# Kernel tuning notes

Hardware: AMD Instinct MI355X
Metric: run time of the kernel (lower is better)

## Reference

```python
import jax, jax.numpy as jnp
import numpy as np

N = 50000  # num_nodes
K_DIFF = 2  # max_diffusion_step


def _spmm(rows, cols, vals, x):
    # sparse (N,N) @ dense (N,F): y[r] += v * x[c]
    return jax.ops.segment_sum(vals[:, None] * x[cols], rows, num_segments=N)


def setup_inputs() -> dict:
    key = jax.random.key(0)
    ks = jax.random.split(key, 9)
    B, D, O, E = 8, 64, 64, 1600000
    num_matrices = 2 * K_DIFF + 1
    return {
        "x": jax.random.normal(ks[0], (B, N, D), dtype=jnp.float32),
        "rows0": jax.random.randint(ks[1], (E,), 0, N),
        "cols0": jax.random.randint(ks[2], (E,), 0, N),
        "vals0": jax.random.uniform(ks[3], (E,), dtype=jnp.float32),
        "rows1": jax.random.randint(ks[4], (E,), 0, N),
        "cols1": jax.random.randint(ks[5], (E,), 0, N),
        "vals1": jax.random.uniform(ks[6], (E,), dtype=jnp.float32),
        "weight": jax.random.normal(ks[7], (D * num_matrices, O), dtype=jnp.float32) * 0.1,
        "biases": jnp.zeros((O,), dtype=jnp.float32),
    }


def reference(x, rows0, cols0, vals0, rows1, cols1, vals1, weight, biases):
    B, n, D = x.shape
    # 'b n d -> n (b d)'
    x0 = jnp.transpose(x, (1, 0, 2)).reshape(n, B * D)
    xs = [x0]
    for (r, c, v) in ((rows0, cols0, vals0), (rows1, cols1, vals1)):
        x1 = _spmm(r, c, v, x0)
        xs.append(x1)
        x_prev, x_curr = x0, x1
        for _ in range(2, K_DIFF + 1):
            x_next = 2.0 * _spmm(r, c, v, x_curr) - x_prev
            xs.append(x_next)
            x_prev, x_curr = x_curr, x_next
    Km = len(xs)
    xk = jnp.stack(xs, axis=0).reshape(Km, n, B, D)  # k n b d
    # 'k n (b d) -> b n d k' then '(b n)(d k)'
    feat = jnp.transpose(xk, (2, 1, 3, 0)).reshape(B * n, D * Km)
    out = feat @ weight + biases
    return out.reshape(B, n, -1)
```

## Files before the change

kernel.cpp:

```cpp
#include <hip/hip_runtime.h>

#define N_NODES 50000
#define BDIM 8
#define DDIM 64
#define ODIM 64
#define KM 5
#define BD 512
#define CAP 72
#define CAPL 76
#define YSTR 88
#define SCHUNKS 8
#define CROWS (N_NODES / SCHUNKS)
#define SLICES 8
#define SFEAT 64
#define RBLK_H ((N_NODES + 31) / 32)

typedef unsigned int u32;
typedef unsigned short u16;

typedef __attribute__((ext_vector_type(8))) short short8;
typedef __attribute__((ext_vector_type(4))) float f32x4;

__device__ __forceinline__ u16 pack1(float f) {
  u32 a = __float_as_uint(f);
  return (u16)((a + 0x7FFFu + ((a >> 16) & 1u)) >> 16);
}
__device__ __forceinline__ u32 pack2(float f0, float f1) {
  return (u32)pack1(f0) | ((u32)pack1(f1) << 16);
}
__device__ __forceinline__ float bfl(u32 u) { return __uint_as_float(u << 16); }
__device__ __forceinline__ float bfh(u32 u) { return __uint_as_float(u & 0xFFFF0000u); }

__device__ __forceinline__ int wave_max(int v) {
  v = max(v, __shfl_xor(v, 8));
  v = max(v, __shfl_xor(v, 16));
  v = max(v, __shfl_xor(v, 32));
  return v;
}

__global__ void k_transpose_h(const float* __restrict__ x, u16* __restrict__ x0h, int tot4) {
  int i = blockIdx.x * blockDim.x + threadIdx.x;
  if (i >= tot4) return;
  int f = i << 2;
  int d = f & (DDIM - 1);
  int nb = f >> 6;
  int b = nb / N_NODES;
  int n = nb - b * N_NODES;
  float4 v = *(const float4*)(x + (size_t)f);
  uint2 w = make_uint2(pack2(v.x, v.y), pack2(v.z, v.w));
  *(uint2*)(x0h + (size_t)n * BD + b * DDIM + d) = w;
}

__global__ void __launch_bounds__(256) k_scatter_cap(
    const int* __restrict__ r0, const int* __restrict__ c0, const float* __restrict__ v0,
    const int* __restrict__ r1, const int* __restrict__ c1, const float* __restrict__ v1,
    int* __restrict__ cnt , u32* __restrict__ cv , int E4, int bpc) {
  int chunk = blockIdx.x / bpc;
  int i = (blockIdx.x - chunk * bpc) * blockDim.x + threadIdx.x;
  int lo = chunk * CROWS;
  const int* rr; const int* cc; const float* vv; int base, j;
  if (i < E4) { rr = r0; cc = c0; vv = v0; base = 0; j = i; }
  else if (i < 2 * E4) { rr = r1; cc = c1; vv = v1; base = N_NODES; j = i - E4; }
  else return;
  int4 r = *(const int4*)(rr + (size_t)j * 4);
  int4 c = *(const int4*)(cc + (size_t)j * 4);
  float4 v = *(const float4*)(vv + (size_t)j * 4);
  int p;
  if ((u32)(r.x - lo) < CROWS) {
    p = atomicAdd(&cnt[base + r.x], 1);
    if (p < CAP) cv[(size_t)(base + r.x) * CAP + p] = (u32)c.x | ((u32)pack1(v.x) << 16);
  }
  if ((u32)(r.y - lo) < CROWS) {
    p = atomicAdd(&cnt[base + r.y], 1);
    if (p < CAP) cv[(size_t)(base + r.y) * CAP + p] = (u32)c.y | ((u32)pack1(v.y) << 16);
  }
  if ((u32)(r.z - lo) < CROWS) {
    p = atomicAdd(&cnt[base + r.z], 1);
    if (p < CAP) cv[(size_t)(base + r.z) * CAP + p] = (u32)c.z | ((u32)pack1(v.z) << 16);
  }
  if ((u32)(r.w - lo) < CROWS) {
    p = atomicAdd(&cnt[base + r.w], 1);
    if (p < CAP) cv[(size_t)(base + r.w) * CAP + p] = (u32)c.w | ((u32)pack1(v.w) << 16);
  }
}

__global__ void k_prep_w(const float* __restrict__ weight, u16* __restrict__ wfrag) {
  for (int i = threadIdx.x; i < 2560; i += 256) {
    int lane = i & 63;
    int ob = (i >> 6) & 3;
    int half = (i >> 8) & 1;
    int k = i >> 9;
    int o = ob * 16 + (lane & 15);
    #pragma unroll
    for (int j = 0; j < 8; ++j) {
      int d = half * 32 + ((lane >> 4) * 8) + j;
      wfrag[(size_t)i * 8 + j] = pack1(weight[(d * KM + k) * ODIM + o]);
    }
  }
}

__device__ __forceinline__ const short8* wfp(const u16* __restrict__ wfrag,
                                             int k, int h, int ob, int lane) {
  return (const short8*)(wfrag + (size_t)((((k * 2 + h) * 4 + ob) * 64 + lane) * 8));
}

__device__ __forceinline__ void fma8(float a[8], uint4 q, float v) {
  a[0] = fmaf(v, bfl(q.x), a[0]); a[1] = fmaf(v, bfh(q.x), a[1]);
  a[2] = fmaf(v, bfl(q.y), a[2]); a[3] = fmaf(v, bfh(q.y), a[3]);
  a[4] = fmaf(v, bfl(q.z), a[4]); a[5] = fmaf(v, bfh(q.z), a[5]);
  a[6] = fmaf(v, bfl(q.w), a[6]); a[7] = fmaf(v, bfh(q.w), a[7]);
}

__device__ __forceinline__ void gather_lds(const u32* __restrict__ cvp ,
                                           const u16* __restrict__ xb,
                                           int n, int nmax, float acc[8]) {
  float A0[8] = {}, A1[8] = {}, A2[8] = {}, A3[8] = {};
  int e = 0;
  for (; e + 4 <= nmax; e += 4) {
    uint4 q = *(const uint4*)(cvp + e);
    u32 q0 = (e + 0 < n) ? q.x : 0u;
    u32 q1 = (e + 1 < n) ? q.y : 0u;
    u32 q2 = (e + 2 < n) ? q.z : 0u;
    u32 q3 = (e + 3 < n) ? q.w : 0u;
    uint4 d0 = *(const uint4*)(xb + (size_t)(q0 & 0xFFFFu) * BD);
    uint4 d1 = *(const uint4*)(xb + (size_t)(q1 & 0xFFFFu) * BD);
    uint4 d2 = *(const uint4*)(xb + (size_t)(q2 & 0xFFFFu) * BD);
    uint4 d3 = *(const uint4*)(xb + (size_t)(q3 & 0xFFFFu) * BD);
    fma8(A0, d0, bfh(q0));
    fma8(A1, d1, bfh(q1));
    fma8(A2, d2, bfh(q2));
    fma8(A3, d3, bfh(q3));
  }
  for (; e < nmax; ++e) {
    u32 q = (e < n) ? cvp[e] : 0u;
    uint4 d = *(const uint4*)(xb + (size_t)(q & 0xFFFFu) * BD);
    fma8(A0, d, bfh(q));
  }
  #pragma unroll
  for (int j = 0; j < 8; ++j) acc[j] = (A0[j] + A1[j]) + (A2[j] + A3[j]);
}

template<int G>
__device__ __forceinline__ void stage_cv(const int* __restrict__ cnt, const u32* __restrict__ cv,
                                         int rbase, u32* __restrict__ cvl, int* __restrict__ nn) {
  if (threadIdx.x < 32 * G) {
    int g = threadIdx.x >> 5, i2 = threadIdx.x & 31;
    int node = rbase + i2;
    nn[threadIdx.x] = (node < N_NODES) ? min(cnt[g * N_NODES + node], CAP) : 0;
  }
  const int QR = CAP / 4;
  for (int idx = threadIdx.x; idx < G * 32 * QR; idx += 256) {
    int g = idx / (32 * QR);
    int rem = idx - g * (32 * QR);
    int i2 = rem / QR, w = rem - i2 * QR;
    int node = rbase + i2;
    uint4 q = (node < N_NODES)
        ? *(const uint4*)(cv + (size_t)(g * N_NODES + node) * CAP + w * 4)
        : make_uint4(0, 0, 0, 0);
    *(uint4*)(&cvl[(g * 32 + i2) * CAPL + w * 4]) = q;
  }
  __syncthreads();
}

__global__ void __launch_bounds__(256, 4) k_hop1f(const int* __restrict__ cnt,
                                                  const u32* __restrict__ cv,
                                                  const u16* __restrict__ x0h,
                                                  const u16* __restrict__ wfrag,
                                                  const float* __restrict__ bias,
                                                  u16* __restrict__ slabA0,
                                                  u16* __restrict__ slabA1,
                                                  float* __restrict__ out) {
  __shared__ u32 cvl[2 * 32 * CAPL];
  __shared__ int nn[64];
  const int sid = blockIdx.x / RBLK_H;
  const int rbase = (blockIdx.x - sid * RBLK_H) * 32;
  stage_cv<2>(cnt, cv, rbase, cvl, nn);

  const int wid = threadIdx.x >> 6, lane = threadIdx.x & 63;
  const int gi = lane >> 3, pe = lane & 7;
  const int i2 = wid * 8 + gi;
  const int node = rbase + i2;
  const bool nv = node < N_NODES;
  const int n0 = nn[i2], n1 = nn[32 + i2];
  const int m0 = wave_max(n0), m1 = wave_max(n1);
  const u32* cvp0 = &cvl[i2 * CAPL];
  const u32* cvp1 = &cvl[(32 + i2) * CAPL];

  const int t = wid >> 1, obp = (wid & 1) * 2;
  const int ar = lane & 15, kg = lane >> 4, col = lane & 15;
  const int anode = min(rbase + t * 16 + ar, N_NODES - 1);
  const float bv0 = bias[obp * 16 + col];
  const float bv1 = bias[(obp + 1) * 16 + col];

  for (int s = sid * 4; s < sid * 4 + 4; ++s) {
    const u16* xb = x0h + s * SFEAT + pe * 8;
    float y0[8], y1[8];
    gather_lds(cvp0, xb, n0, m0, y0);
    gather_lds(cvp1, xb, n1, m1, y1);
    if (nv) {
      size_t doff = (size_t)node * BD + s * SFEAT + pe * 8;
      *(uint4*)(slabA0 + doff) = make_uint4(pack2(y0[0], y0[1]), pack2(y0[2], y0[3]),
                                            pack2(y0[4], y0[5]), pack2(y0[6], y0[7]));
      *(uint4*)(slabA1 + doff) = make_uint4(pack2(y1[0], y1[1]), pack2(y1[2], y1[3]),
                                            pack2(y1[4], y1[5]), pack2(y1[6], y1[7]));
    }
    f32x4 acc0 = {0.f, 0.f, 0.f, 0.f}, acc1 = {0.f, 0.f, 0.f, 0.f};
    #pragma unroll
    for (int h = 0; h < 2; ++h) {
      short8 a = *(const short8*)(x0h + (size_t)anode * BD + s * SFEAT + h * 32 + kg * 8);
      acc0 = __builtin_amdgcn_mfma_f32_16x16x32_bf16(a, *wfp(wfrag, 0, h, obp, lane), acc0, 0, 0, 0);
      acc1 = __builtin_amdgcn_mfma_f32_16x16x32_bf16(a, *wfp(wfrag, 0, h, obp + 1, lane), acc1, 0, 0, 0);
    }
    #pragma unroll
    for (int reg = 0; reg < 4; ++reg) {
      int onode = rbase + t * 16 + kg * 4 + reg;
      if (onode < N_NODES) {
        size_t ob_ = ((size_t)s * N_NODES + onode) * ODIM;
        out[ob_ + obp * 16 + col] = acc0[reg] + bv0;
        out[ob_ + (obp + 1) * 16 + col] = acc1[reg] + bv1;
      }
    }
  }
}

template<int KSELF, int KY>
__global__ void __launch_bounds__(256, 4) k_hop2(const int* __restrict__ cnt_g,
                                                 const u32* __restrict__ cv_g,
                                                 const u16* __restrict__ srcslab,
                                                 const u16* __restrict__ x0h,
                                                 const u16* __restrict__ wfrag,
                                                 float* __restrict__ out) {
  __shared__ u32 cvl[32 * CAPL];
  __shared__ int nn[32];
  __shared__ u16 ytile[32 * YSTR];
  const int sid = blockIdx.x / RBLK_H;
  const int rbase = (blockIdx.x - sid * RBLK_H) * 32;
  stage_cv<1>(cnt_g, cv_g, rbase, cvl, nn);

  const int wid = threadIdx.x >> 6, lane = threadIdx.x & 63;
  const int gi = lane >> 3, pe = lane & 7;
  const int i2 = wid * 8 + gi;
  const int node = rbase + i2;
  const int nsafe = min(node, N_NODES - 1);
  const int n = nn[i2];
  const int m = wave_max(n);
  const u32* cvp = &cvl[i2 * CAPL];

  const int t = wid >> 1, obp = (wid & 1) * 2;
  const int ar = lane & 15, kg = lane >> 4, col = lane & 15;
  const int anode = min(rbase + t * 16 + ar, N_NODES - 1);

  for (int s = sid * 4; s < sid * 4 + 4; ++s) {
    const u16* xb = srcslab + s * SFEAT + pe * 8;
    float y[8];
    gather_lds(cvp, xb, n, m, y);
    {
      uint4 qp = *(const uint4*)(x0h + (size_t)nsafe * BD + s * SFEAT + pe * 8);
      float p[8] = {bfl(qp.x), bfh(qp.x), bfl(qp.y), bfh(qp.y),
                    bfl(qp.z), bfh(qp.z), bfl(qp.w), bfh(qp.w)};
      #pragma unroll
      for (int j = 0; j < 8; ++j) y[j] = 2.f * y[j] - p[j];
    }
    *(uint4*)(&ytile[i2 * YSTR + pe * 8]) =
        make_uint4(pack2(y[0], y[1]), pack2(y[2], y[3]),
                   pack2(y[4], y[5]), pack2(y[6], y[7]));
    __syncthreads();
    f32x4 acc0 = {0.f, 0.f, 0.f, 0.f}, acc1 = {0.f, 0.f, 0.f, 0.f};
    #pragma unroll
    for (int h = 0; h < 2; ++h) {
      short8 aS = *(const short8*)(srcslab + (size_t)anode * BD + s * SFEAT + h * 32 + kg * 8);
      short8 aY = *(const short8*)(&ytile[(t * 16 + ar) * YSTR + h * 32 + kg * 8]);
      acc0 = __builtin_amdgcn_mfma_f32_16x16x32_bf16(aS, *wfp(wfrag, KSELF, h, obp, lane), acc0, 0, 0, 0);
      acc1 = __builtin_amdgcn_mfma_f32_16x16x32_bf16(aS, *wfp(wfrag, KSELF, h, obp + 1, lane), acc1, 0, 0, 0);
      acc0 = __builtin_amdgcn_mfma_f32_16x16x32_bf16(aY, *wfp(wfrag, KY, h, obp, lane), acc0, 0, 0, 0);
      acc1 = __builtin_amdgcn_mfma_f32_16x16x32_bf16(aY, *wfp(wfrag, KY, h, obp + 1, lane), acc1, 0, 0, 0);
    }
    #pragma unroll
    for (int reg = 0; reg < 4; ++reg) {
      int onode = rbase + t * 16 + kg * 4 + reg;
      if (onode < N_NODES) {
        size_t ob_ = ((size_t)s * N_NODES + onode) * ODIM;
        out[ob_ + obp * 16 + col] += acc0[reg];
        out[ob_ + (obp + 1) * 16 + col] += acc1[reg];
      }
    }
    __syncthreads();
  }
}

extern "C" void kernel_launch(void* const* d_in, const int* in_sizes, int n_in,
                              void* d_out, int out_size, void* d_ws, size_t ws_size,
                              hipStream_t stream) {
  const float* x      = (const float*)d_in[0];
  const int*   rows0  = (const int*)d_in[1];
  const int*   cols0  = (const int*)d_in[2];
  const float* vals0  = (const float*)d_in[3];
  const int*   rows1  = (const int*)d_in[4];
  const int*   cols1  = (const int*)d_in[5];
  const float* vals1  = (const float*)d_in[6];
  const float* weight = (const float*)d_in[7];
  const float* bias   = (const float*)d_in[8];
  float* out = (float*)d_out;
  const int E = in_sizes[1];
  const int E4 = E >> 2;

  char* p = (char*)d_ws;
  auto alloc = [&](size_t bytes) {
    char* q = p;
    p += (bytes + 255) & ~(size_t)255;
    return q;
  };
  u16* x0h    = (u16*)alloc((size_t)N_NODES * BD * sizeof(u16));
  u16* slabA0 = (u16*)alloc((size_t)N_NODES * BD * sizeof(u16));
  u16* slabA1 = (u16*)alloc((size_t)N_NODES * BD * sizeof(u16));
  int* cnt    = (int*)alloc((size_t)2 * N_NODES * sizeof(int));
  u32* cv     = (u32*)alloc((size_t)2 * N_NODES * CAP * sizeof(u32));
  u16* wfrag  = (u16*)alloc((size_t)2560 * 8 * sizeof(u16));
  if ((size_t)(p - (char*)d_ws) > ws_size) return;

  const int tot4 = BDIM * N_NODES * DDIM / 4;
  k_transpose_h<<<(tot4 + 255) / 256, 256, 0, stream>>>(x, x0h, tot4);

  (void)hipMemsetAsync(cnt, 0, (size_t)2 * N_NODES * sizeof(int), stream);
  const int bpc = (2 * E4 + 255) / 256;
  k_scatter_cap<<<SCHUNKS * bpc, 256, 0, stream>>>(rows0, cols0, vals0,
                                                   rows1, cols1, vals1,
                                                   cnt, cv, E4, bpc);
  k_prep_w<<<1, 256, 0, stream>>>(weight, wfrag);

  k_hop1f<<<2 * RBLK_H, 256, 0, stream>>>(cnt, cv, x0h, wfrag, bias, slabA0, slabA1, out);
  k_hop2<1, 2><<<2 * RBLK_H, 256, 0, stream>>>(cnt, cv, slabA0, x0h, wfrag, out);
  k_hop2<3, 4><<<2 * RBLK_H, 256, 0, stream>>>(cnt + N_NODES, cv + (size_t)N_NODES * CAP,
                                               slabA1, x0h, wfrag, out);
}
```

Baseline: 1.063 ms.

## Split first-hop gather into 16 per-slice launches over a sliced x0 layout

```diff
diff --git a/kernel.cpp b/kernel.cpp
--- a/kernel.cpp
+++ b/kernel.cpp
@@ -11,15 +11,18 @@
 #define YSTR 88
 #define SCHUNKS 8
 #define CROWS (N_NODES / SCHUNKS)
-#define SLICES 8
 #define SFEAT 64
+#define SF32 32
+#define NERA 16
 #define RBLK_H ((N_NODES + 31) / 32)
 
 typedef unsigned int u32;
 typedef unsigned short u16;
+typedef unsigned long long u64;
 
 typedef __attribute__((ext_vector_type(8))) short short8;
 typedef __attribute__((ext_vector_type(4))) float f32x4;
+typedef __attribute__((ext_vector_type(4))) unsigned int u32x4;
 
 __device__ __forceinline__ u16 pack1(float f) {
   u32 a = __float_as_uint(f);
@@ -38,7 +41,7 @@
   return v;
 }
 
-__global__ void k_transpose_h(const float* __restrict__ x, u16* __restrict__ x0h, int tot4) {
+__global__ void k_transpose_h(const float* __restrict__ x, u16* __restrict__ x0sl, int tot4) {
   int i = blockIdx.x * blockDim.x + threadIdx.x;
   if (i >= tot4) return;
   int f = i << 2;
@@ -46,9 +49,11 @@
   int nb = f >> 6;
   int b = nb / N_NODES;
   int n = nb - b * N_NODES;
+  int s = b * 2 + (d >> 5);
+  int fo = d & 31;
   float4 v = *(const float4*)(x + (size_t)f);
   uint2 w = make_uint2(pack2(v.x, v.y), pack2(v.z, v.w));
-  *(uint2*)(x0h + (size_t)n * BD + b * DDIM + d) = w;
+  *(uint2*)(x0sl + ((size_t)s * N_NODES + n) * SF32 + fo) = w;
 }
 
 __global__ void __launch_bounds__(256) k_scatter_cap(
@@ -140,6 +145,34 @@
   for (int j = 0; j < 8; ++j) acc[j] = (A0[j] + A1[j]) + (A2[j] + A3[j]);
 }
 
+__device__ __forceinline__ void fma4(float a[4], uint2 q, float v) {
+  a[0] = fmaf(v, bfl(q.x), a[0]); a[1] = fmaf(v, bfh(q.x), a[1]);
+  a[2] = fmaf(v, bfl(q.y), a[2]); a[3] = fmaf(v, bfh(q.y), a[3]);
+}
+
+__device__ __forceinline__ void gather4(const u32* __restrict__ cvp ,
+                                        const u16* __restrict__ xb,
+                                        int n, int nmax, float acc[4]) {
+  float A0[4] = {}, A1[4] = {}, A2[4] = {}, A3[4] = {};
+  for (int e = 0; e < nmax; e += 4) {
+    uint4 q = *(const uint4*)(cvp + e);
+    u32 q0 = (e + 0 < n) ? q.x : 0u;
+    u32 q1 = (e + 1 < n) ? q.y : 0u;
+    u32 q2 = (e + 2 < n) ? q.z : 0u;
+    u32 q3 = (e + 3 < n) ? q.w : 0u;
+    uint2 d0 = *(const uint2*)(xb + (size_t)(q0 & 0xFFFFu) * SF32);
+    uint2 d1 = *(const uint2*)(xb + (size_t)(q1 & 0xFFFFu) * SF32);
+    uint2 d2 = *(const uint2*)(xb + (size_t)(q2 & 0xFFFFu) * SF32);
+    uint2 d3 = *(const uint2*)(xb + (size_t)(q3 & 0xFFFFu) * SF32);
+    fma4(A0, d0, bfh(q0));
+    fma4(A1, d1, bfh(q1));
+    fma4(A2, d2, bfh(q2));
+    fma4(A3, d3, bfh(q3));
+  }
+  #pragma unroll
+  for (int j = 0; j < 4; ++j) acc[j] = (A0[j] + A1[j]) + (A2[j] + A3[j]);
+}
+
 template<int G>
 __device__ __forceinline__ void stage_cv(const int* __restrict__ cnt, const u32* __restrict__ cv,
                                          int rbase, u32* __restrict__ cvl, int* __restrict__ nn) {
@@ -148,87 +181,62 @@
     int node = rbase + i2;
     nn[threadIdx.x] = (node < N_NODES) ? min(cnt[g * N_NODES + node], CAP) : 0;
   }
+  __syncthreads();
   const int QR = CAP / 4;
   for (int idx = threadIdx.x; idx < G * 32 * QR; idx += 256) {
     int g = idx / (32 * QR);
     int rem = idx - g * (32 * QR);
     int i2 = rem / QR, w = rem - i2 * QR;
-    int node = rbase + i2;
-    uint4 q = (node < N_NODES)
-        ? *(const uint4*)(cv + (size_t)(g * N_NODES + node) * CAP + w * 4)
-        : make_uint4(0, 0, 0, 0);
-    *(uint4*)(&cvl[(g * 32 + i2) * CAPL + w * 4]) = q;
+    if (w * 4 < nn[g * 32 + i2]) {
+      int node = rbase + i2;
+      u32x4 q = __builtin_nontemporal_load(
+          (const u32x4*)(cv + (size_t)(g * N_NODES + node) * CAP + w * 4));
+      *(u32x4*)(&cvl[(g * 32 + i2) * CAPL + w * 4]) = q;
+    }
   }
   __syncthreads();
 }
 
-__global__ void __launch_bounds__(256, 4) k_hop1f(const int* __restrict__ cnt,
-                                                  const u32* __restrict__ cv,
-                                                  const u16* __restrict__ x0h,
-                                                  const u16* __restrict__ wfrag,
-                                                  const float* __restrict__ bias,
-                                                  u16* __restrict__ slabA0,
-                                                  u16* __restrict__ slabA1,
-                                                  float* __restrict__ out) {
+__global__ void __launch_bounds__(256, 8) k_gath_era(const int* __restrict__ cnt,
+                                                     const u32* __restrict__ cv,
+                                                     const u16* __restrict__ x0sl,
+                                                     u16* __restrict__ slabA0,
+                                                     u16* __restrict__ slabA1,
+                                                     int s) {
   __shared__ u32 cvl[2 * 32 * CAPL];
   __shared__ int nn[64];
-  const int sid = blockIdx.x / RBLK_H;
-  const int rbase = (blockIdx.x - sid * RBLK_H) * 32;
+  const int rbase = blockIdx.x * 32;
   stage_cv<2>(cnt, cv, rbase, cvl, nn);
 
   const int wid = threadIdx.x >> 6, lane = threadIdx.x & 63;
   const int gi = lane >> 3, pe = lane & 7;
   const int i2 = wid * 8 + gi;
   const int node = rbase + i2;
-  const bool nv = node < N_NODES;
   const int n0 = nn[i2], n1 = nn[32 + i2];
   const int m0 = wave_max(n0), m1 = wave_max(n1);
   const u32* cvp0 = &cvl[i2 * CAPL];
   const u32* cvp1 = &cvl[(32 + i2) * CAPL];
 
-  const int t = wid >> 1, obp = (wid & 1) * 2;
-  const int ar = lane & 15, kg = lane >> 4, col = lane & 15;
-  const int anode = min(rbase + t * 16 + ar, N_NODES - 1);
-  const float bv0 = bias[obp * 16 + col];
-  const float bv1 = bias[(obp + 1) * 16 + col];
-
-  for (int s = sid * 4; s < sid * 4 + 4; ++s) {
-    const u16* xb = x0h + s * SFEAT + pe * 8;
-    float y0[8], y1[8];
-    gather_lds(cvp0, xb, n0, m0, y0);
-    gather_lds(cvp1, xb, n1, m1, y1);
-    if (nv) {
-      size_t doff = (size_t)node * BD + s * SFEAT + pe * 8;
-      *(uint4*)(slabA0 + doff) = make_uint4(pack2(y0[0], y0[1]), pack2(y0[2], y0[3]),
-                                            pack2(y0[4], y0[5]), pack2(y0[6], y0[7]));
-      *(uint4*)(slabA1 + doff) = make_uint4(pack2(y1[0], y1[1]), pack2(y1[2], y1[3]),
-                                            pack2(y1[4], y1[5]), pack2(y1[6], y1[7]));
-    }
-    f32x4 acc0 = {0.f, 0.f, 0.f, 0.f}, acc1 = {0.f, 0.f, 0.f, 0.f};
-    #pragma unroll
-    for (int h = 0; h < 2; ++h) {
-      short8 a = *(const short8*)(x0h + (size_t)anode * BD + s * SFEAT + h * 32 + kg * 8);
-      acc0 = __builtin_amdgcn_mfma_f32_16x16x32_bf16(a, *wfp(wfrag, 0, h, obp, lane), acc0, 0, 0, 0);
-      acc1 = __builtin_amdgcn_mfma_f32_16x16x32_bf16(a, *wfp(wfrag, 0, h, obp + 1, lane), acc1, 0, 0, 0);
-    }
-    #pragma unroll
-    for (int reg = 0; reg < 4; ++reg) {
-      int onode = rbase + t * 16 + kg * 4 + reg;
-      if (onode < N_NODES) {
-        size_t ob_ = ((size_t)s * N_NODES + onode) * ODIM;
-        out[ob_ + obp * 16 + col] = acc0[reg] + bv0;
-        out[ob_ + (obp + 1) * 16 + col] = acc1[reg] + bv1;
-      }
-    }
-  }
-}
-
-template<int KSELF, int KY>
+  const u16* xb = x0sl + (size_t)s * N_NODES * SF32 + pe * 4;
+  float y0[4], y1[4];
+  gather4(cvp0, xb, n0, m0, y0);
+  gather4(cvp1, xb, n1, m1, y1);
+  if (node < N_NODES) {
+    size_t doff = (size_t)node * BD + s * SF32 + pe * 4;
+    u64 s0 = (u64)pack2(y0[0], y0[1]) | ((u64)pack2(y0[2], y0[3]) << 32);
+    u64 s1 = (u64)pack2(y1[0], y1[1]) | ((u64)pack2(y1[2], y1[3]) << 32);
+    __builtin_nontemporal_store(s0, (u64*)(slabA0 + doff));
+    __builtin_nontemporal_store(s1, (u64*)(slabA1 + doff));
+  }
+}
+
+template<int KSELF, int KY, bool FIRST>
 __global__ void __launch_bounds__(256, 4) k_hop2(const int* __restrict__ cnt_g,
                                                  const u32* __restrict__ cv_g,
                                                  const u16* __restrict__ srcslab,
-                                                 const u16* __restrict__ x0h,
+                                                 const u16* __restrict__ x0sl,
                                                  const u16* __restrict__ wfrag,
+                                                 const float* __restrict__ bias,
                                                  float* __restrict__ out) {
   __shared__ u32 cvl[32 * CAPL];
   __shared__ int nn[32];
@@ -249,13 +257,18 @@
   const int t = wid >> 1, obp = (wid & 1) * 2;
   const int ar = lane & 15, kg = lane >> 4, col = lane & 15;
   const int anode = min(rbase + t * 16 + ar, N_NODES - 1);
+  const float bv0 = bias[obp * 16 + col];
+  const float bv1 = bias[(obp + 1) * 16 + col];
+
+  const int ec_h = pe >> 2;
+  const int ec_off = (pe & 3) * 8;
 
   for (int s = sid * 4; s < sid * 4 + 4; ++s) {
     const u16* xb = srcslab + s * SFEAT + pe * 8;
     float y[8];
     gather_lds(cvp, xb, n, m, y);
     {
-      uint4 qp = *(const uint4*)(x0h + (size_t)nsafe * BD + s * SFEAT + pe * 8);
+      uint4 qp = *(const uint4*)(x0sl + ((size_t)(2 * s + ec_h) * N_NODES + nsafe) * SF32 + ec_off);
       float p[8] = {bfl(qp.x), bfh(qp.x), bfl(qp.y), bfh(qp.y),
                     bfl(qp.z), bfh(qp.z), bfl(qp.w), bfh(qp.w)};
       #pragma unroll
@@ -274,14 +287,24 @@
       acc1 = __builtin_amdgcn_mfma_f32_16x16x32_bf16(aS, *wfp(wfrag, KSELF, h, obp + 1, lane), acc1, 0, 0, 0);
       acc0 = __builtin_amdgcn_mfma_f32_16x16x32_bf16(aY, *wfp(wfrag, KY, h, obp, lane), acc0, 0, 0, 0);
       acc1 = __builtin_amdgcn_mfma_f32_16x16x32_bf16(aY, *wfp(wfrag, KY, h, obp + 1, lane), acc1, 0, 0, 0);
+      if (FIRST) {
+        short8 a0f = *(const short8*)(x0sl + ((size_t)(2 * s + h) * N_NODES + anode) * SF32 + kg * 8);
+        acc0 = __builtin_amdgcn_mfma_f32_16x16x32_bf16(a0f, *wfp(wfrag, 0, h, obp, lane), acc0, 0, 0, 0);
+        acc1 = __builtin_amdgcn_mfma_f32_16x16x32_bf16(a0f, *wfp(wfrag, 0, h, obp + 1, lane), acc1, 0, 0, 0);
+      }
     }
     #pragma unroll
     for (int reg = 0; reg < 4; ++reg) {
       int onode = rbase + t * 16 + kg * 4 + reg;
       if (onode < N_NODES) {
         size_t ob_ = ((size_t)s * N_NODES + onode) * ODIM;
-        out[ob_ + obp * 16 + col] += acc0[reg];
-        out[ob_ + (obp + 1) * 16 + col] += acc1[reg];
+        if (FIRST) {
+          out[ob_ + obp * 16 + col] = acc0[reg] + bv0;
+          out[ob_ + (obp + 1) * 16 + col] = acc1[reg] + bv1;
+        } else {
+          out[ob_ + obp * 16 + col] += acc0[reg];
+          out[ob_ + (obp + 1) * 16 + col] += acc1[reg];
+        }
       }
     }
     __syncthreads();
@@ -310,7 +333,7 @@
     p += (bytes + 255) & ~(size_t)255;
     return q;
   };
-  u16* x0h    = (u16*)alloc((size_t)N_NODES * BD * sizeof(u16));
+  u16* x0sl   = (u16*)alloc((size_t)N_NODES * BD * sizeof(u16));
   u16* slabA0 = (u16*)alloc((size_t)N_NODES * BD * sizeof(u16));
   u16* slabA1 = (u16*)alloc((size_t)N_NODES * BD * sizeof(u16));
   int* cnt    = (int*)alloc((size_t)2 * N_NODES * sizeof(int));
@@ -319,7 +342,7 @@
   if ((size_t)(p - (char*)d_ws) > ws_size) return;
 
   const int tot4 = BDIM * N_NODES * DDIM / 4;
-  k_transpose_h<<<(tot4 + 255) / 256, 256, 0, stream>>>(x, x0h, tot4);
+  k_transpose_h<<<(tot4 + 255) / 256, 256, 0, stream>>>(x, x0sl, tot4);
 
   (void)hipMemsetAsync(cnt, 0, (size_t)2 * N_NODES * sizeof(int), stream);
   const int bpc = (2 * E4 + 255) / 256;
@@ -328,8 +351,10 @@
                                                    cnt, cv, E4, bpc);
   k_prep_w<<<1, 256, 0, stream>>>(weight, wfrag);
 
-  k_hop1f<<<2 * RBLK_H, 256, 0, stream>>>(cnt, cv, x0h, wfrag, bias, slabA0, slabA1, out);
-  k_hop2<1, 2><<<2 * RBLK_H, 256, 0, stream>>>(cnt, cv, slabA0, x0h, wfrag, out);
-  k_hop2<3, 4><<<2 * RBLK_H, 256, 0, stream>>>(cnt + N_NODES, cv + (size_t)N_NODES * CAP,
-                                               slabA1, x0h, wfrag, out);
-}
+  for (int s = 0; s < NERA; ++s)
+    k_gath_era<<<RBLK_H, 256, 0, stream>>>(cnt, cv, x0sl, slabA0, slabA1, s);
+
+  k_hop2<1, 2, true><<<2 * RBLK_H, 256, 0, stream>>>(cnt, cv, slabA0, x0sl, wfrag, bias, out);
+  k_hop2<3, 4, false><<<2 * RBLK_H, 256, 0, stream>>>(cnt + N_NODES, cv + (size_t)N_NODES * CAP,
+                                                      slabA1, x0sl, wfrag, bias, out);
+}
```

New measurement: 1.098 ms. 1.03x slower.
